# Kernel optimization log

Measured on AMD Instinct MI355X. Metric: run time of the kernel, lower is better.

## Reference

```python
import jax, jax.numpy as jnp
import numpy as np

B, N, G, K, V = 4, 512, 8, 64, 32000


def setup_inputs() -> dict:
    key = jax.random.key(0)
    k1, k2, k3 = jax.random.split(key, 3)
    phi = jax.random.normal(k1, (B, N, G, K), dtype=jnp.float32)
    # psi initialized uniform(-0.5, 0.5) as in torch.nn.init.uniform_
    psi = jax.random.uniform(k2, (V, K), dtype=jnp.float32, minval=-0.5, maxval=0.5)
    # perm[h, v] = index of h^{-1} acting on vocab word v (data-dependent permutation)
    perm = jax.random.randint(k3, (G, V), 0, V, dtype=jnp.int64)
    return {"phi": phi, "psi": psi, "perm": perm}


def reference(phi, psi, perm):
    # For each group element h: logits[b,n,v] += dot(phi[b,n,h,:], psi[perm[h,v],:])
    # Gather psi rows per group element: [G, V, K]
    psi_g = psi[perm]
    logits = jnp.einsum("bnhk,hvk->bnv", phi, psi_g)  # [B, N, V]
    return jax.nn.softmax(logits, axis=-1)
```

## Files before the change

### kernel.cpp

```cpp
#include <hip/hip_runtime.h>
#include <math.h>


#define M_ROWS 2048
#define V_DIM  32000
#define C_DIM  512
#define G_DIM  8
#define K_DIM  64
#define BM     128
#define BV     128
#define BK     32
#define NVBLK  (V_DIM / BV)
#define NMT    (M_ROWS / BM)
#define NKT    (C_DIM / BK)
#define NSEG   25
#define SEGV   (NVBLK / NSEG)
#define LDSBUF 12288
#define LDS_ROW 40

typedef _Float16 f16x8 __attribute__((ext_vector_type(8)));
typedef _Float16 f16x4 __attribute__((ext_vector_type(4)));
typedef float    f32x4 __attribute__((ext_vector_type(4)));


__device__ __forceinline__ void gl_lds16(const void* g, void* l) {
  __builtin_amdgcn_global_load_lds(
      (const __attribute__((address_space(1))) unsigned int*)g,
      (__attribute__((address_space(3))) unsigned int*)l, 16, 0, 0);
}

__global__ __launch_bounds__(256) void gdecode_prep_phi(
    const float* __restrict__ phi, _Float16* __restrict__ aws)
{
  const int ga   = blockIdx.x * 256 + threadIdx.x;
  const int g    = ga & 511;
  const int half = (ga >> 9) & 1;
  const int tile = ga >> 10;
  const int kq = g >> 7, r = g & 127;
  const int m  = (tile >> 4) * BM + r;
  const int k  = (tile & 15) * BK + kq * 8;
  const float4 x0 = *(const float4*)(phi + (size_t)m * C_DIM + k);
  const float4 x1 = *(const float4*)(phi + (size_t)m * C_DIM + k + 4);
  const float xs[8] = {x0.x, x0.y, x0.z, x0.w, x1.x, x1.y, x1.z, x1.w};
  f16x8 o;
  #pragma unroll
  for (int j = 0; j < 8; ++j) {
    _Float16 hi = (_Float16)xs[j];
    o[j] = half ? (_Float16)(xs[j] - (float)hi) : hi;
  }
  *(f16x8*)(aws + (size_t)ga * 8) = o;
}

__global__ __launch_bounds__(256) void gdecode_prep_psi(
    const float* __restrict__ psi, const int* __restrict__ perm, const int pstride,
    _Float16* __restrict__ bws)
{
  const int gb   = blockIdx.x * 256 + threadIdx.x;
  const int g    = gb & 511;
  const int tile = gb >> 9;
  const int it = tile / 250;
  const int vb = tile - it * 250;
  const int kq = g >> 7, r = g & 127;
  const int h   = it >> 1;
  const int kin = (it & 1) * 32 + kq * 8;
  const int v   = vb * BV + r;
  const int pr  = perm[(size_t)(h * V_DIM + v) * pstride];
  const float4 x0 = *(const float4*)(psi + (size_t)pr * K_DIM + kin);
  const float4 x1 = *(const float4*)(psi + (size_t)pr * K_DIM + kin + 4);
  f16x8 o = {(_Float16)x0.x, (_Float16)x0.y, (_Float16)x0.z, (_Float16)x0.w,
             (_Float16)x1.x, (_Float16)x1.y, (_Float16)x1.z, (_Float16)x1.w};
  *(f16x8*)(bws + (size_t)gb * 8) = o;
}

__global__ __launch_bounds__(256, 4) void gdecode_gemm2(
    const _Float16* __restrict__ aws, const _Float16* __restrict__ bws,
    float* __restrict__ out, float* __restrict__ smax, float* __restrict__ ssum)
{
  __shared__ __align__(16) _Float16 lds[2 * LDSBUF];

  const int b   = blockIdx.x;
  const int xcd = b & 7;
  const int i   = b >> 3;
  const int mt  = i >> 5;
  const int vb  = xcd * 32 + (i & 31);
  if (vb >= NVBLK) return;

  const int vbase = vb * BV;
  const int mbase = mt * BM;

  const int t    = threadIdx.x;
  const int wid  = t >> 6;
  const int lane = t & 63;
  const int wm   = wid & 1;
  const int wv   = wid >> 1;
  const int lrow = lane & 15;
  const int quad = lane >> 4;

  const _Float16* gA = aws + (size_t)mt * NKT * 2 * 4096;
  const _Float16* gB = bws + (size_t)vb * 4096;

  auto STAGE = [&](int it, _Float16* dst) {
    const _Float16* ga = gA + (size_t)it * 2 * 4096;
    const _Float16* gb = gB + (size_t)it * NVBLK * 4096;
    gl_lds16(ga + (size_t)t * 8,          dst + t * 8);
    gl_lds16(ga + 2048 + (size_t)t * 8,   dst + 2048 + t * 8);
    gl_lds16(ga + 4096 + (size_t)t * 8,   dst + 4096 + t * 8);
    gl_lds16(ga + 6144 + (size_t)t * 8,   dst + 6144 + t * 8);
    gl_lds16(gb + (size_t)t * 8,          dst + 8192 + t * 8);
    gl_lds16(gb + 2048 + (size_t)t * 8,   dst + 8192 + 2048 + t * 8);
  };

  f32x4 acc[4][4] = {};

  STAGE(0, lds);
  STAGE(1, lds + LDSBUF);

  #pragma unroll 2
  for (int it = 0; it < 16; ++it) {
    _Float16* cur = lds + (it & 1) * LDSBUF;

    if (it < 15) asm volatile("s_waitcnt vmcnt(6)" ::: "memory");
    else         asm volatile("s_waitcnt vmcnt(0)" ::: "memory");
    __builtin_amdgcn_s_barrier();

    const _Float16* sAh = cur;
    const _Float16* sAl = cur + 4096;
    const _Float16* sB  = cur + 8192;

    f16x8 ah[4], al[4], bf[4];
    #pragma unroll
    for (int k = 0; k < 4; ++k) {
      const int ra = quad * 1024 + (wm * 64 + k * 16 + lrow) * 8;
      const int rb = quad * 1024 + (wv * 64 + k * 16 + lrow) * 8;
      ah[k] = *(const f16x8*)(sAh + ra);
      al[k] = *(const f16x8*)(sAl + ra);
      bf[k] = *(const f16x8*)(sB + rb);
    }
    #pragma unroll
    for (int k = 0; k < 4; ++k) {
      #pragma unroll
      for (int j = 0; j < 4; ++j) {
        acc[k][j] = __builtin_amdgcn_mfma_f32_16x16x32_f16(ah[k], bf[j], acc[k][j], 0, 0, 0);
        acc[k][j] = __builtin_amdgcn_mfma_f32_16x16x32_f16(al[k], bf[j], acc[k][j], 0, 0, 0);
      }
    }
    asm volatile("s_waitcnt lgkmcnt(0)" ::: "memory");
    __builtin_amdgcn_s_barrier();
    if (it < 14) STAGE(it + 2, cur);
  }

  float* redmax = (float*)lds;
  float* redsum = redmax + 2 * BM;
  const int rowb = wm * 64;

  #pragma unroll
  for (int k = 0; k < 4; ++k) {
    #pragma unroll
    for (int r = 0; r < 4; ++r) {
      float v = fmaxf(fmaxf(acc[k][0][r], acc[k][1][r]),
                      fmaxf(acc[k][2][r], acc[k][3][r]));
      v = fmaxf(v, __shfl_xor(v, 1));
      v = fmaxf(v, __shfl_xor(v, 2));
      v = fmaxf(v, __shfl_xor(v, 4));
      v = fmaxf(v, __shfl_xor(v, 8));
      if (lrow == 0) redmax[(rowb + k * 16 + quad * 4 + r) * 2 + wv] = v;
    }
  }
  __syncthreads();
  float gmx[4][4];
  #pragma unroll
  for (int k = 0; k < 4; ++k) {
    #pragma unroll
    for (int r = 0; r < 4; ++r) {
      int row = rowb + k * 16 + quad * 4 + r;
      gmx[k][r] = fmaxf(redmax[row * 2], redmax[row * 2 + 1]);
    }
  }
  #pragma unroll
  for (int k = 0; k < 4; ++k) {
    #pragma unroll
    for (int r = 0; r < 4; ++r) {
      float s = __expf(acc[k][0][r] - gmx[k][r]) + __expf(acc[k][1][r] - gmx[k][r])
              + __expf(acc[k][2][r] - gmx[k][r]) + __expf(acc[k][3][r] - gmx[k][r]);
      s += __shfl_xor(s, 1);
      s += __shfl_xor(s, 2);
      s += __shfl_xor(s, 4);
      s += __shfl_xor(s, 8);
      if (lrow == 0) redsum[(rowb + k * 16 + quad * 4 + r) * 2 + wv] = s;
    }
  }
  __syncthreads();
  if (t < BM) {
    size_t o = (size_t)vb * M_ROWS + mbase + t;
    smax[o] = fmaxf(redmax[t * 2], redmax[t * 2 + 1]);
    ssum[o] = redsum[t * 2] + redsum[t * 2 + 1];
  }
  #pragma unroll
  for (int k = 0; k < 4; ++k) {
    #pragma unroll
    for (int j = 0; j < 4; ++j) {
      #pragma unroll
      for (int r = 0; r < 4; ++r) {
        int grow = mbase + rowb + k * 16 + quad * 4 + r;
        int gcol = vbase + wv * 64 + j * 16 + lrow;
        __builtin_nontemporal_store(acc[k][j][r], out + (size_t)grow * V_DIM + gcol);
      }
    }
  }
}

__global__ __launch_bounds__(256) void gdecode_combine1(
    const float* __restrict__ smax, const float* __restrict__ ssum,
    float* __restrict__ pmax, float* __restrict__ psum)
{
  const int seg = blockIdx.x % NSEG;
  const int m   = (blockIdx.x / NSEG) * 256 + threadIdx.x;
  float Mv = -3.4e38f;
  #pragma unroll
  for (int j = 0; j < SEGV; ++j)
    Mv = fmaxf(Mv, smax[(size_t)(seg * SEGV + j) * M_ROWS + m]);
  float S = 0.f;
  #pragma unroll
  for (int j = 0; j < SEGV; ++j) {
    const size_t o = (size_t)(seg * SEGV + j) * M_ROWS + m;
    S += ssum[o] * __expf(smax[o] - Mv);
  }
  pmax[(size_t)seg * M_ROWS + m] = Mv;
  psum[(size_t)seg * M_ROWS + m] = S;
}

__global__ __launch_bounds__(256) void gdecode_norm(
    float* __restrict__ out, const float* __restrict__ pmax, const float* __restrict__ psum)
{
  const int m = blockIdx.x >> 2;
  const int c = blockIdx.x & 3;
  float Mv = -3.4e38f;
  #pragma unroll
  for (int s = 0; s < NSEG; ++s) Mv = fmaxf(Mv, pmax[(size_t)s * M_ROWS + m]);
  float S = 0.f;
  #pragma unroll
  for (int s = 0; s < NSEG; ++s)
    S += psum[(size_t)s * M_ROWS + m] * __expf(pmax[(size_t)s * M_ROWS + m] - Mv);
  const float Iv = 1.f / S;

  f32x4* row = (f32x4*)(out + (size_t)m * V_DIM + c * 8000);
  for (int i = threadIdx.x; i < 2000; i += 256) {
    f32x4 x = __builtin_nontemporal_load(row + i);
    f32x4 y;
    y[0] = __expf(x[0] - Mv) * Iv;
    y[1] = __expf(x[1] - Mv) * Iv;
    y[2] = __expf(x[2] - Mv) * Iv;
    y[3] = __expf(x[3] - Mv) * Iv;
    __builtin_nontemporal_store(y, row + i);
  }
}


__global__ __launch_bounds__(256, 2) void gdecode_gemm_fb(
    const float* __restrict__ phi, const float* __restrict__ psi,
    const int* __restrict__ perm, const int pstride,
    float* __restrict__ out, float* __restrict__ smax, float* __restrict__ ssum)
{
  __shared__ __align__(16) _Float16 lds[3 * BM * LDS_ROW];
  _Float16* sAhi = lds;
  _Float16* sAlo = lds + BM * LDS_ROW;
  _Float16* sB   = lds + 2 * BM * LDS_ROW;

  const int t     = threadIdx.x;
  const int vbase = blockIdx.x * BV;
  const int mbase = blockIdx.y * BM;

  const int kg = t & 7;
  const int r0 = t >> 3;

  const int wid  = t >> 6;
  const int lane = t & 63;
  const int wm   = wid & 1;
  const int wv   = wid >> 1;
  const int lrow = lane & 15;
  const int quad = lane >> 4;

  f32x4 acc[4][4] = {};

  for (int it = 0; it < 16; ++it) {
    const int cb  = it * BK;
    const int h   = cb >> 6;
    const int kin = cb & 63;

    float4 av[4], bv[4];
    #pragma unroll
    for (int i = 0; i < 4; ++i) {
      int m = r0 + i * 32;
      av[i] = *(const float4*)(phi + (size_t)(mbase + m) * C_DIM + cb + kg * 4);
    }
    #pragma unroll
    for (int i = 0; i < 4; ++i) {
      int v  = r0 + i * 32;
      int pr = perm[(size_t)(h * V_DIM + vbase + v) * pstride];
      bv[i]  = *(const float4*)(psi + (size_t)pr * K_DIM + kin + kg * 4);
    }

    __syncthreads();

    #pragma unroll
    for (int i = 0; i < 4; ++i) {
      int m = r0 + i * 32;
      float4 x = av[i];
      _Float16 h0 = (_Float16)x.x, h1 = (_Float16)x.y,
               h2 = (_Float16)x.z, h3 = (_Float16)x.w;
      f16x4 hi = {h0, h1, h2, h3};
      f16x4 lo = {(_Float16)(x.x - (float)h0), (_Float16)(x.y - (float)h1),
                  (_Float16)(x.z - (float)h2), (_Float16)(x.w - (float)h3)};
      *(f16x4*)(sAhi + m * LDS_ROW + kg * 4) = hi;
      *(f16x4*)(sAlo + m * LDS_ROW + kg * 4) = lo;
    }
    #pragma unroll
    for (int i = 0; i < 4; ++i) {
      int v = r0 + i * 32;
      float4 x = bv[i];
      f16x4 w = {(_Float16)x.x, (_Float16)x.y, (_Float16)x.z, (_Float16)x.w};
      *(f16x4*)(sB + v * LDS_ROW + kg * 4) = w;
    }

    __syncthreads();

    f16x8 ah[4], al[4], bf[4];
    #pragma unroll
    for (int i = 0; i < 4; ++i) {
      ah[i] = *(const f16x8*)(sAhi + (wm * 64 + i * 16 + lrow) * LDS_ROW + quad * 8);
      al[i] = *(const f16x8*)(sAlo + (wm * 64 + i * 16 + lrow) * LDS_ROW + quad * 8);
      bf[i] = *(const f16x8*)(sB   + (wv * 64 + i * 16 + lrow) * LDS_ROW + quad * 8);
    }
    #pragma unroll
    for (int i = 0; i < 4; ++i) {
      #pragma unroll
      for (int j = 0; j < 4; ++j) {
        acc[i][j] = __builtin_amdgcn_mfma_f32_16x16x32_f16(ah[i], bf[j], acc[i][j], 0, 0, 0);
        acc[i][j] = __builtin_amdgcn_mfma_f32_16x16x32_f16(al[i], bf[j], acc[i][j], 0, 0, 0);
      }
    }
  }

  __syncthreads();
  float* redmax = (float*)lds;
  float* redsum = redmax + 2 * BM;
  const int rowb = wm * 64;

  #pragma unroll
  for (int i = 0; i < 4; ++i) {
    #pragma unroll
    for (int r = 0; r < 4; ++r) {
      float v = fmaxf(fmaxf(acc[i][0][r], acc[i][1][r]),
                      fmaxf(acc[i][2][r], acc[i][3][r]));
      v = fmaxf(v, __shfl_xor(v, 1));
      v = fmaxf(v, __shfl_xor(v, 2));
      v = fmaxf(v, __shfl_xor(v, 4));
      v = fmaxf(v, __shfl_xor(v, 8));
      if (lrow == 0) redmax[(rowb + i * 16 + quad * 4 + r) * 2 + wv] = v;
    }
  }
  __syncthreads();
  float gmx[4][4];
  #pragma unroll
  for (int i = 0; i < 4; ++i) {
    #pragma unroll
    for (int r = 0; r < 4; ++r) {
      int row = rowb + i * 16 + quad * 4 + r;
      gmx[i][r] = fmaxf(redmax[row * 2], redmax[row * 2 + 1]);
    }
  }
  #pragma unroll
  for (int i = 0; i < 4; ++i) {
    #pragma unroll
    for (int r = 0; r < 4; ++r) {
      float s = __expf(acc[i][0][r] - gmx[i][r]) + __expf(acc[i][1][r] - gmx[i][r])
              + __expf(acc[i][2][r] - gmx[i][r]) + __expf(acc[i][3][r] - gmx[i][r]);
      s += __shfl_xor(s, 1);
      s += __shfl_xor(s, 2);
      s += __shfl_xor(s, 4);
      s += __shfl_xor(s, 8);
      if (lrow == 0) redsum[(rowb + i * 16 + quad * 4 + r) * 2 + wv] = s;
    }
  }
  __syncthreads();
  if (smax != nullptr && t < BM) {
    int row = t;
    size_t o = (size_t)(mbase + row) * NVBLK + blockIdx.x;
    smax[o] = fmaxf(redmax[row * 2], redmax[row * 2 + 1]);
    ssum[o] = redsum[row * 2] + redsum[row * 2 + 1];
  }
  #pragma unroll
  for (int i = 0; i < 4; ++i) {
    #pragma unroll
    for (int j = 0; j < 4; ++j) {
      #pragma unroll
      for (int r = 0; r < 4; ++r) {
        int grow = mbase + rowb + i * 16 + quad * 4 + r;
        int gcol = vbase + wv * 64 + j * 16 + lrow;
        out[(size_t)grow * V_DIM + gcol] = acc[i][j][r];
      }
    }
  }
}

__global__ __launch_bounds__(256) void gdecode_softmax_ws(
    float* __restrict__ out, const float* __restrict__ smax, const float* __restrict__ ssum)
{
  __shared__ float sbuf[4];
  const int m = blockIdx.x;
  const int t = threadIdx.x;
  const float* rm = smax + (size_t)m * NVBLK;
  const float* rs = ssum + (size_t)m * NVBLK;

  float lm = -3.4e38f;
  for (int i = t; i < NVBLK; i += 256) lm = fmaxf(lm, rm[i]);
  for (int d = 1; d < 64; d <<= 1) lm = fmaxf(lm, __shfl_xor(lm, d));
  if ((t & 63) == 0) sbuf[t >> 6] = lm;
  __syncthreads();
  const float M = fmaxf(fmaxf(sbuf[0], sbuf[1]), fmaxf(sbuf[2], sbuf[3]));
  __syncthreads();

  float ls = 0.f;
  for (int i = t; i < NVBLK; i += 256) ls += rs[i] * __expf(rm[i] - M);
  for (int d = 1; d < 64; d <<= 1) ls += __shfl_xor(ls, d);
  if ((t & 63) == 0) sbuf[t >> 6] = ls;
  __syncthreads();
  const float inv = 1.f / (sbuf[0] + sbuf[1] + sbuf[2] + sbuf[3]);

  float4* row = (float4*)(out + (size_t)m * V_DIM);
  for (int i = t; i < V_DIM / 4; i += 256) {
    float4 x = row[i];
    x.x = __expf(x.x - M) * inv;
    x.y = __expf(x.y - M) * inv;
    x.z = __expf(x.z - M) * inv;
    x.w = __expf(x.w - M) * inv;
    row[i] = x;
  }
}

__global__ __launch_bounds__(256) void gdecode_softmax_nows(float* __restrict__ out)
{
  __shared__ float sbuf[4];
  const int m = blockIdx.x;
  const int t = threadIdx.x;
  float4* row = (float4*)(out + (size_t)m * V_DIM);

  float lm = -3.4e38f;
  for (int i = t; i < V_DIM / 4; i += 256) {
    float4 x = row[i];
    lm = fmaxf(lm, fmaxf(fmaxf(x.x, x.y), fmaxf(x.z, x.w)));
  }
  for (int d = 1; d < 64; d <<= 1) lm = fmaxf(lm, __shfl_xor(lm, d));
  if ((t & 63) == 0) sbuf[t >> 6] = lm;
  __syncthreads();
  const float M = fmaxf(fmaxf(sbuf[0], sbuf[1]), fmaxf(sbuf[2], sbuf[3]));
  __syncthreads();

  float ls = 0.f;
  for (int i = t; i < V_DIM / 4; i += 256) {
    float4 x = row[i];
    ls += __expf(x.x - M) + __expf(x.y - M) + __expf(x.z - M) + __expf(x.w - M);
  }
  for (int d = 1; d < 64; d <<= 1) ls += __shfl_xor(ls, d);
  if ((t & 63) == 0) sbuf[t >> 6] = ls;
  __syncthreads();
  const float inv = 1.f / (sbuf[0] + sbuf[1] + sbuf[2] + sbuf[3]);

  for (int i = t; i < V_DIM / 4; i += 256) {
    float4 x = row[i];
    x.x = __expf(x.x - M) * inv;
    x.y = __expf(x.y - M) * inv;
    x.z = __expf(x.z - M) * inv;
    x.w = __expf(x.w - M) * inv;
    row[i] = x;
  }
}


extern "C" void kernel_launch(void* const* d_in, const int* in_sizes, int n_in,
                              void* d_out, int out_size, void* d_ws, size_t ws_size,
                              hipStream_t stream)
{
  const float* phi  = (const float*)d_in[0];
  const float* psi  = (const float*)d_in[1];
  const int*   perm = (const int*)d_in[2];
  const int pstride = (in_sizes[2] == 2 * G_DIM * V_DIM) ? 2 : 1;

  float* out = (float*)d_out;

  const size_t AWS_B  = (size_t)NMT * NKT * 2 * 4096 * 2;
  const size_t BWS_B  = (size_t)NKT * NVBLK * 4096 * 2;
  const size_t STAT_B = (size_t)NVBLK * M_ROWS * 4;
  const size_t PART_B = (size_t)NSEG * M_ROWS * 4;
  const size_t need_fast = AWS_B + BWS_B + 2 * STAT_B + 2 * PART_B;

  if (d_ws != nullptr && ws_size >= need_fast) {
    char* wp = (char*)d_ws;
    _Float16* aws = (_Float16*)wp;                 wp += AWS_B;
    _Float16* bws = (_Float16*)wp;                 wp += BWS_B;
    float* smax   = (float*)wp;                    wp += STAT_B;
    float* ssum   = (float*)wp;                    wp += STAT_B;
    float* pmax   = (float*)wp;                    wp += PART_B;
    float* psum   = (float*)wp;

    gdecode_prep_phi<<<(NMT * NKT * 2 * 512) / 256, 256, 0, stream>>>(phi, aws);
    gdecode_prep_psi<<<(NKT * NVBLK * 512) / 256, 256, 0, stream>>>(psi, perm, pstride, bws);

    gdecode_gemm2<<<4096, 256, 0, stream>>>(aws, bws, out, smax, ssum);

    gdecode_combine1<<<NSEG * (M_ROWS / 256), 256, 0, stream>>>(smax, ssum, pmax, psum);
    gdecode_norm<<<M_ROWS * 4, 256, 0, stream>>>(out, pmax, psum);
    return;
  }

  const size_t need_old = (size_t)M_ROWS * NVBLK * 2 * sizeof(float);
  const bool hasws = (d_ws != nullptr) && (ws_size >= need_old);
  float* smax = hasws ? (float*)d_ws : nullptr;
  float* ssum = hasws ? smax + (size_t)M_ROWS * NVBLK : nullptr;

  dim3 grid(NVBLK, M_ROWS / BM);
  gdecode_gemm_fb<<<grid, 256, 0, stream>>>(phi, psi, perm, pstride, out, smax, ssum);

  if (hasws)
    gdecode_softmax_ws<<<M_ROWS, 256, 0, stream>>>(out, smax, ssum);
  else
    gdecode_softmax_nows<<<M_ROWS, 256, 0, stream>>>(out);
}
```

Measured before the change: 543.8 us.

## Merge prep kernels, coalesce psi gather, simplify GEMM double-buffer pipeline

Merges the phi and psi prep kernels into one launch and remaps psi threads so each group of eight threads reads one full gathered psi row, which coalesces the permuted gather. The GEMM main loop drops the explicit vmcnt/lgkmcnt waits and two-stage prefetch in favour of a one-ahead prefetch with __syncthreads, giving simpler but shallower latency hiding. The norm kernel switches from nontemporal to ordinary loads. These are several unrelated changes with opposing likely effects.

New measurement: 537.4 us. Within noise of the previous version (-1.2%).

```diff
diff --git a/kernel.cpp b/kernel.cpp
--- a/kernel.cpp
+++ b/kernel.cpp
@@ -16,6 +16,8 @@
 #define NSEG   25
 #define SEGV   (NVBLK / NSEG)
 #define LDSBUF 12288
+#define PSI_BLKS 8000
+#define PHI_BLKS 1024
 #define LDS_ROW 40
 
 typedef _Float16 f16x8 __attribute__((ext_vector_type(8)));
@@ -29,47 +31,47 @@
       (__attribute__((address_space(3))) unsigned int*)l, 16, 0, 0);
 }
 
-__global__ __launch_bounds__(256) void gdecode_prep_phi(
-    const float* __restrict__ phi, _Float16* __restrict__ aws)
-{
-  const int ga   = blockIdx.x * 256 + threadIdx.x;
-  const int g    = ga & 511;
-  const int half = (ga >> 9) & 1;
-  const int tile = ga >> 10;
-  const int kq = g >> 7, r = g & 127;
-  const int m  = (tile >> 4) * BM + r;
-  const int k  = (tile & 15) * BK + kq * 8;
-  const float4 x0 = *(const float4*)(phi + (size_t)m * C_DIM + k);
-  const float4 x1 = *(const float4*)(phi + (size_t)m * C_DIM + k + 4);
-  const float xs[8] = {x0.x, x0.y, x0.z, x0.w, x1.x, x1.y, x1.z, x1.w};
-  f16x8 o;
-  #pragma unroll
-  for (int j = 0; j < 8; ++j) {
-    _Float16 hi = (_Float16)xs[j];
-    o[j] = half ? (_Float16)(xs[j] - (float)hi) : hi;
-  }
-  *(f16x8*)(aws + (size_t)ga * 8) = o;
-}
-
-__global__ __launch_bounds__(256) void gdecode_prep_psi(
-    const float* __restrict__ psi, const int* __restrict__ perm, const int pstride,
-    _Float16* __restrict__ bws)
-{
-  const int gb   = blockIdx.x * 256 + threadIdx.x;
-  const int g    = gb & 511;
-  const int tile = gb >> 9;
-  const int it = tile / 250;
-  const int vb = tile - it * 250;
-  const int kq = g >> 7, r = g & 127;
-  const int h   = it >> 1;
-  const int kin = (it & 1) * 32 + kq * 8;
-  const int v   = vb * BV + r;
-  const int pr  = perm[(size_t)(h * V_DIM + v) * pstride];
-  const float4 x0 = *(const float4*)(psi + (size_t)pr * K_DIM + kin);
-  const float4 x1 = *(const float4*)(psi + (size_t)pr * K_DIM + kin + 4);
-  f16x8 o = {(_Float16)x0.x, (_Float16)x0.y, (_Float16)x0.z, (_Float16)x0.w,
-             (_Float16)x1.x, (_Float16)x1.y, (_Float16)x1.z, (_Float16)x1.w};
-  *(f16x8*)(bws + (size_t)gb * 8) = o;
+__global__ __launch_bounds__(256) void gdecode_prep(
+    const float* __restrict__ phi, const float* __restrict__ psi,
+    const int* __restrict__ perm, const int pstride,
+    _Float16* __restrict__ aws, _Float16* __restrict__ bws)
+{
+  const int b = blockIdx.x;
+  const int t = threadIdx.x;
+  if (b < PSI_BLKS) {
+    const int h   = b / 1000;
+    const int vg  = b - h * 1000;
+    const int v   = vg * 32 + (t >> 3);
+    const int kq8 = t & 7;
+    const int pr  = perm[(size_t)(h * V_DIM + v) * pstride];
+    const float4 x0 = *(const float4*)(psi + (size_t)pr * K_DIM + kq8 * 8);
+    const float4 x1 = *(const float4*)(psi + (size_t)pr * K_DIM + kq8 * 8 + 4);
+    f16x8 o = {(_Float16)x0.x, (_Float16)x0.y, (_Float16)x0.z, (_Float16)x0.w,
+               (_Float16)x1.x, (_Float16)x1.y, (_Float16)x1.z, (_Float16)x1.w};
+    const int it = 2 * h + (kq8 >> 2);
+    const int kq = kq8 & 3;
+    const int vb = v >> 7;
+    const int r  = v & 127;
+    *(f16x8*)(bws + ((((size_t)it * NVBLK + vb) * 4 + kq) * 128 + r) * 8) = o;
+  } else {
+    const int ga   = (b - PSI_BLKS) * 256 + t;
+    const int g    = ga & 511;
+    const int half = (ga >> 9) & 1;
+    const int tile = ga >> 10;
+    const int kq = g >> 7, r = g & 127;
+    const int m  = (tile >> 4) * BM + r;
+    const int k  = (tile & 15) * BK + kq * 8;
+    const float4 x0 = *(const float4*)(phi + (size_t)m * C_DIM + k);
+    const float4 x1 = *(const float4*)(phi + (size_t)m * C_DIM + k + 4);
+    const float xs[8] = {x0.x, x0.y, x0.z, x0.w, x1.x, x1.y, x1.z, x1.w};
+    f16x8 o;
+    #pragma unroll
+    for (int j = 0; j < 8; ++j) {
+      _Float16 hi = (_Float16)xs[j];
+      o[j] = half ? (_Float16)(xs[j] - (float)hi) : hi;
+    }
+    *(f16x8*)(aws + (size_t)ga * 8) = o;
+  }
 }
 
 __global__ __launch_bounds__(256, 4) void gdecode_gemm2(
@@ -113,15 +115,11 @@
   f32x4 acc[4][4] = {};
 
   STAGE(0, lds);
-  STAGE(1, lds + LDSBUF);
-
-  #pragma unroll 2
+  __syncthreads();
+
   for (int it = 0; it < 16; ++it) {
     _Float16* cur = lds + (it & 1) * LDSBUF;
-
-    if (it < 15) asm volatile("s_waitcnt vmcnt(6)" ::: "memory");
-    else         asm volatile("s_waitcnt vmcnt(0)" ::: "memory");
-    __builtin_amdgcn_s_barrier();
+    if (it < 15) STAGE(it + 1, lds + ((it & 1) ^ 1) * LDSBUF);
 
     const _Float16* sAh = cur;
     const _Float16* sAl = cur + 4096;
@@ -144,9 +142,7 @@
         acc[k][j] = __builtin_amdgcn_mfma_f32_16x16x32_f16(al[k], bf[j], acc[k][j], 0, 0, 0);
       }
     }
-    asm volatile("s_waitcnt lgkmcnt(0)" ::: "memory");
-    __builtin_amdgcn_s_barrier();
-    if (it < 14) STAGE(it + 2, cur);
+    __syncthreads();
   }
 
   float* redmax = (float*)lds;
@@ -245,7 +241,7 @@
 
   f32x4* row = (f32x4*)(out + (size_t)m * V_DIM + c * 8000);
   for (int i = threadIdx.x; i < 2000; i += 256) {
-    f32x4 x = __builtin_nontemporal_load(row + i);
+    f32x4 x = row[i];
     f32x4 y;
     y[0] = __expf(x[0] - Mv) * Iv;
     y[1] = __expf(x[1] - Mv) * Iv;
@@ -503,8 +499,7 @@
     float* pmax   = (float*)wp;                    wp += PART_B;
     float* psum   = (float*)wp;
 
-    gdecode_prep_phi<<<(NMT * NKT * 2 * 512) / 256, 256, 0, stream>>>(phi, aws);
-    gdecode_prep_psi<<<(NKT * NVBLK * 512) / 256, 256, 0, stream>>>(psi, perm, pstride, bws);
+    gdecode_prep<<<PSI_BLKS + PHI_BLKS, 256, 0, stream>>>(phi, psi, perm, pstride, aws, bws);
 
     gdecode_gemm2<<<4096, 256, 0, stream>>>(aws, bws, out, smax, ssum);
 
```
